# Kernel tuning notes

Measured on AMD Instinct MI355X. Metric: run time of the kernel, lower is better.

## Reference

```python
import jax, jax.numpy as jnp
import numpy as np

B, T, D, P = 32, 512, 256, 8
MEL_MAX = T * (P - 1)  # 3584, worst-case expanded length


def setup_inputs() -> dict:
    key = jax.random.key(0)
    k0, k1, k2 = jax.random.split(key, 3)
    x = jax.random.normal(k0, (B, T, D), dtype=jnp.float32)
    # Xavier-uniform-ish scaled weights
    W1 = jax.random.normal(k1, (D, D), dtype=jnp.float32) * (1.0 / np.sqrt(D))
    b1 = jnp.zeros((D,), dtype=jnp.float32)
    W2 = jax.random.normal(k2, (P, D), dtype=jnp.float32) * (1.0 / np.sqrt(D))
    b2 = jnp.zeros((P,), dtype=jnp.float32)
    return {"x": x, "W1": W1, "b1": b1, "W2": W2, "b2": b2,
            "mel_max_length": MEL_MAX}


def reference(x, W1, b1, W2, b2, mel_max_length):
    # DurationPredictor: Linear -> ReLU -> Linear -> softmax
    h = jax.nn.relu(jnp.einsum('btd,ed->bte', x, W1) + b1)
    P_probs = jax.nn.softmax(jnp.einsum('btd,pd->btp', h, W2) + b2, axis=-1)
    # transfer (eval): duration = argmax over class dim
    dur = jnp.argmax(P_probs, axis=-1)  # [B,T] ints in [0, P-1]; alpha=1.0
    # Vectorized LR/expand: frame t maps to the token whose cumulative
    # duration interval contains t.
    cs = jnp.cumsum(dur, axis=1)                 # [B,T] inclusive cumsum
    total = cs[:, -1]                            # [B] mel lengths
    t = jnp.arange(mel_max_length)               # [M]
    src = jax.vmap(lambda c: jnp.searchsorted(c, t, side='right'))(cs)  # [B,M]
    src = jnp.minimum(src, x.shape[1] - 1)
    out = jnp.take_along_axis(x, src[..., None], axis=1)  # [B,M,D]
    mask = (t[None, :] < total[:, None])[..., None]       # pad beyond length
    return jnp.where(mask, out, jnp.zeros((), dtype=x.dtype))
```

## Files before the change

### kernel.cpp

```cpp
#include <hip/hip_runtime.h>

#define B_ 32
#define T_ 512
#define D_ 256
#define P_ 8
#define BT (B_*T_)
#define ROWS 32
#define KT 32
#define NKT (D_/KT)

typedef float f4 __attribute__((ext_vector_type(4)));

__global__ void k_transpose(const float* __restrict__ W1, float* __restrict__ w1t) {
  int d = blockIdx.x;
  int e = threadIdx.x;
  w1t[d * D_ + e] = W1[e * D_ + d];
}

__global__ __launch_bounds__(256, 2) void k_dur(
    const float* __restrict__ x, const float* __restrict__ w1t,
    const float* __restrict__ b1, const float* __restrict__ W2,
    const float* __restrict__ b2, int* __restrict__ dur)
{
  __shared__ float xs[ROWS][D_];
  __shared__ float wst[KT][D_];

  const int tid  = threadIdx.x;
  const int lane = tid & 63;
  const int wave = tid >> 6;
  const int row0 = blockIdx.x * ROWS;

  for (int i = 0; i < 8; ++i) {
    int r = wave * 8 + i;
    const float* g = x + (size_t)(row0 + r) * D_ + lane * 4;
    __builtin_amdgcn_global_load_lds(
        (const __attribute__((address_space(1))) void*)g,
        (__attribute__((address_space(3))) void*)&xs[r][0], 16, 0, 0);
  }

  f4 b1v = *(const f4*)(b1 + lane * 4);
  f4 acc[8];
  #pragma unroll
  for (int i = 0; i < 8; ++i) acc[i] = b1v;

  for (int kt = 0; kt < NKT; ++kt) {
    for (int i = 0; i < 8; ++i) {
      int dd = wave * 8 + i;
      const float* g = w1t + (size_t)(kt * KT + dd) * D_ + lane * 4;
      __builtin_amdgcn_global_load_lds(
          (const __attribute__((address_space(1))) void*)g,
          (__attribute__((address_space(3))) void*)&wst[dd][0], 16, 0, 0);
    }
    __syncthreads();

    f4 loc[8];
    #pragma unroll
    for (int i = 0; i < 8; ++i) loc[i] = (f4){0.f, 0.f, 0.f, 0.f};

    #pragma unroll
    for (int dq = 0; dq < KT / 4; ++dq) {
      f4 wv[4];
      #pragma unroll
      for (int j = 0; j < 4; ++j) wv[j] = *(const f4*)&wst[dq * 4 + j][lane * 4];
      #pragma unroll
      for (int i = 0; i < 8; ++i) {
        f4 xv = *(const f4*)&xs[wave * 8 + i][kt * KT + dq * 4];
        loc[i] += xv.x * wv[0];
        loc[i] += xv.y * wv[1];
        loc[i] += xv.z * wv[2];
        loc[i] += xv.w * wv[3];
      }
    }
    #pragma unroll
    for (int i = 0; i < 8; ++i) acc[i] += loc[i];
    __syncthreads();
  }

  #pragma unroll
  for (int i = 0; i < 8; ++i)
    #pragma unroll
    for (int c = 0; c < 4; ++c) acc[i][c] = fmaxf(acc[i][c], 0.f);

  f4 w2r[P_];
  #pragma unroll
  for (int p = 0; p < P_; ++p) w2r[p] = *(const f4*)(W2 + p * D_ + lane * 4);
  float b2r[P_];
  #pragma unroll
  for (int p = 0; p < P_; ++p) b2r[p] = b2[p];

  float v[64];
  #pragma unroll
  for (int r = 0; r < 8; ++r)
    #pragma unroll
    for (int p = 0; p < P_; ++p) {
      f4 h = acc[r];
      v[r * 8 + p] = h[0]*w2r[p][0] + h[1]*w2r[p][1] + h[2]*w2r[p][2] + h[3]*w2r[p][3];
    }

  #pragma unroll
  for (int step = 0; step < 3; ++step) {
    const int s = 1 << step;
    const int half = 32 >> step;
    const bool upper = (lane & s) != 0;
    #pragma unroll
    for (int i = 0; i < half; ++i) {
      float a = v[i], b = v[i + half];
      float send = upper ? a : b;
      float recv = __shfl_xor(send, s, 64);
      v[i] = (upper ? b : a) + recv;
    }
  }
  #pragma unroll
  for (int s = 8; s < 64; s <<= 1)
    #pragma unroll
    for (int i = 0; i < 8; ++i) v[i] += __shfl_xor(v[i], s, 64);

  if (lane < 8) {
    float best = v[0] + b2r[0];
    int am = 0;
    #pragma unroll
    for (int p = 1; p < P_; ++p) {
      float L = v[p] + b2r[p];
      if (L > best) { best = L; am = p; }
    }
    int r = ((lane & 1) << 2) | (lane & 2) | ((lane & 4) >> 2);
    dur[row0 + wave * 8 + r] = am;
  }
}

__global__ void k_scan(const int* __restrict__ dur, int* __restrict__ src, int mel) {
  __shared__ int sh[T_];
  int t = threadIdx.x, b = blockIdx.x;
  int d = dur[b * T_ + t];
  sh[t] = d;
  __syncthreads();
  for (int s = 1; s < T_; s <<= 1) {
    int a = (t >= s) ? sh[t - s] : 0;
    __syncthreads();
    sh[t] += a;
    __syncthreads();
  }
  int cs = sh[t];
  int start = cs - d;
  int total = sh[T_ - 1];
  for (int m = start; m < cs; ++m) src[b * mel + m] = t;
  for (int m = total + t; m < mel; m += T_) src[b * mel + m] = -1;
}

__global__ __launch_bounds__(256) void k_gather(
    const float* __restrict__ x, const int* __restrict__ src,
    float* __restrict__ out, int mel)
{
  int lane = threadIdx.x & 63;
  int wave = threadIdx.x >> 6;
  int m = blockIdx.x * 4 + wave;
  int b = blockIdx.y;
  if (m >= mel) return;
  int s = src[b * mel + m];
  f4 val = {0.f, 0.f, 0.f, 0.f};
  if (s >= 0) val = *(const f4*)(x + ((size_t)b * T_ + s) * D_ + lane * 4);
  *(f4*)(out + ((size_t)b * mel + m) * D_ + lane * 4) = val;
}

extern "C" void kernel_launch(void* const* d_in, const int* in_sizes, int n_in,
                              void* d_out, int out_size, void* d_ws, size_t ws_size,
                              hipStream_t stream) {
  const float* x  = (const float*)d_in[0];
  const float* W1 = (const float*)d_in[1];
  const float* b1 = (const float*)d_in[2];
  const float* W2 = (const float*)d_in[3];
  const float* b2 = (const float*)d_in[4];
  float* out = (float*)d_out;

  int mel = out_size / (B_ * D_);

  float* w1t = (float*)d_ws;
  int*   dur = (int*)((char*)d_ws + D_ * D_ * sizeof(float));
  int*   src = dur + BT;

  k_transpose<<<D_, D_, 0, stream>>>(W1, w1t);
  k_dur<<<BT / ROWS, 256, 0, stream>>>(x, w1t, b1, W2, b2, dur);
  k_scan<<<B_, T_, 0, stream>>>(dur, src, mel);
  k_gather<<<dim3((mel + 3) / 4, B_), 256, 0, stream>>>(x, src, out, mel);
}
```

Baseline: 69.81 us.

## Double-buffer W1 tiles, double rows per block, and use wave-shuffle scan

The duration kernel now processes 64 rows per block (16 per wave) and double-buffers the W1 tile in LDS, prefetching tile kt+2 while computing tile kt with explicit vmcnt waits and raw barriers. This raises weight reuse per LDS load and overlaps global-to-LDS transfers with the FMA loop. Register and LDS use go up (occupancy hint drops to 1 block/CU) and the grid halves to 256 blocks. The scan kernel replaces the LDS Hillis-Steele loop with a wavefront shuffle scan plus a small per-wave sum fix-up, cutting barriers.

After: 203.3 us. 191% more time.

```diff
diff --git a/kernel.cpp b/kernel.cpp
--- a/kernel.cpp
+++ b/kernel.cpp
@@ -5,9 +5,10 @@
 #define D_ 256
 #define P_ 8
 #define BT (B_*T_)
-#define ROWS 32
 #define KT 32
 #define NKT (D_/KT)
+#define RPW 16
+#define RPB 64
 
 typedef float f4 __attribute__((ext_vector_type(4)));
 
@@ -17,54 +18,57 @@
   w1t[d * D_ + e] = W1[e * D_ + d];
 }
 
-__global__ __launch_bounds__(256, 2) void k_dur(
+__global__ __launch_bounds__(256, 1) void k_dur(
     const float* __restrict__ x, const float* __restrict__ w1t,
     const float* __restrict__ b1, const float* __restrict__ W2,
     const float* __restrict__ b2, int* __restrict__ dur)
 {
-  __shared__ float xs[ROWS][D_];
-  __shared__ float wst[KT][D_];
+  __shared__ float xs[RPB][D_];
+  __shared__ float wst[2][KT][D_];
 
   const int tid  = threadIdx.x;
   const int lane = tid & 63;
   const int wave = tid >> 6;
-  const int row0 = blockIdx.x * ROWS;
-
-  for (int i = 0; i < 8; ++i) {
-    int r = wave * 8 + i;
+  const int row0 = blockIdx.x * RPB;
+
+  for (int i = 0; i < RPW; ++i) {
+    int r = wave * RPW + i;
     const float* g = x + (size_t)(row0 + r) * D_ + lane * 4;
     __builtin_amdgcn_global_load_lds(
         (const __attribute__((address_space(1))) void*)g,
         (__attribute__((address_space(3))) void*)&xs[r][0], 16, 0, 0);
   }
-
-  f4 b1v = *(const f4*)(b1 + lane * 4);
-  f4 acc[8];
-  #pragma unroll
-  for (int i = 0; i < 8; ++i) acc[i] = b1v;
-
-  for (int kt = 0; kt < NKT; ++kt) {
+  for (int bu = 0; bu < 2; ++bu)
     for (int i = 0; i < 8; ++i) {
       int dd = wave * 8 + i;
-      const float* g = w1t + (size_t)(kt * KT + dd) * D_ + lane * 4;
+      const float* g = w1t + (size_t)(bu * KT + dd) * D_ + lane * 4;
       __builtin_amdgcn_global_load_lds(
           (const __attribute__((address_space(1))) void*)g,
-          (__attribute__((address_space(3))) void*)&wst[dd][0], 16, 0, 0);
-    }
-    __syncthreads();
-
-    f4 loc[8];
-    #pragma unroll
-    for (int i = 0; i < 8; ++i) loc[i] = (f4){0.f, 0.f, 0.f, 0.f};
+          (__attribute__((address_space(3))) void*)&wst[bu][dd][0], 16, 0, 0);
+    }
+  asm volatile("s_waitcnt vmcnt(8)" ::: "memory");
+  __builtin_amdgcn_s_barrier();
+  __builtin_amdgcn_sched_barrier(0);
+
+  f4 b1v = *(const f4*)(b1 + lane * 4);
+  f4 acc[RPW];
+  #pragma unroll
+  for (int i = 0; i < RPW; ++i) acc[i] = b1v;
+
+  for (int kt = 0; kt < NKT; ++kt) {
+    const int cur = kt & 1;
+    f4 loc[RPW];
+    #pragma unroll
+    for (int i = 0; i < RPW; ++i) loc[i] = (f4){0.f, 0.f, 0.f, 0.f};
 
     #pragma unroll
     for (int dq = 0; dq < KT / 4; ++dq) {
       f4 wv[4];
       #pragma unroll
-      for (int j = 0; j < 4; ++j) wv[j] = *(const f4*)&wst[dq * 4 + j][lane * 4];
-      #pragma unroll
-      for (int i = 0; i < 8; ++i) {
-        f4 xv = *(const f4*)&xs[wave * 8 + i][kt * KT + dq * 4];
+      for (int j = 0; j < 4; ++j) wv[j] = *(const f4*)&wst[cur][dq * 4 + j][lane * 4];
+      #pragma unroll
+      for (int i = 0; i < RPW; ++i) {
+        f4 xv = *(const f4*)&xs[wave * RPW + i][kt * KT + dq * 4];
         loc[i] += xv.x * wv[0];
         loc[i] += xv.y * wv[1];
         loc[i] += xv.z * wv[2];
@@ -72,12 +76,30 @@
       }
     }
     #pragma unroll
-    for (int i = 0; i < 8; ++i) acc[i] += loc[i];
-    __syncthreads();
-  }
-
-  #pragma unroll
-  for (int i = 0; i < 8; ++i)
+    for (int i = 0; i < RPW; ++i) acc[i] += loc[i];
+
+    if (kt < NKT - 1) {
+      __builtin_amdgcn_s_barrier();
+      __builtin_amdgcn_sched_barrier(0);
+      if (kt + 2 < NKT) {
+        for (int i = 0; i < 8; ++i) {
+          int dd = wave * 8 + i;
+          const float* g = w1t + (size_t)((kt + 2) * KT + dd) * D_ + lane * 4;
+          __builtin_amdgcn_global_load_lds(
+              (const __attribute__((address_space(1))) void*)g,
+              (__attribute__((address_space(3))) void*)&wst[cur][dd][0], 16, 0, 0);
+        }
+        asm volatile("s_waitcnt vmcnt(8)" ::: "memory");
+      } else {
+        asm volatile("s_waitcnt vmcnt(0)" ::: "memory");
+      }
+      __builtin_amdgcn_s_barrier();
+      __builtin_amdgcn_sched_barrier(0);
+    }
+  }
+
+  #pragma unroll
+  for (int i = 0; i < RPW; ++i)
     #pragma unroll
     for (int c = 0; c < 4; ++c) acc[i][c] = fmaxf(acc[i][c], 0.f);
 
@@ -88,61 +110,70 @@
   #pragma unroll
   for (int p = 0; p < P_; ++p) b2r[p] = b2[p];
 
-  float v[64];
-  #pragma unroll
-  for (int r = 0; r < 8; ++r)
-    #pragma unroll
-    for (int p = 0; p < P_; ++p) {
-      f4 h = acc[r];
-      v[r * 8 + p] = h[0]*w2r[p][0] + h[1]*w2r[p][1] + h[2]*w2r[p][2] + h[3]*w2r[p][3];
-    }
-
-  #pragma unroll
-  for (int step = 0; step < 3; ++step) {
-    const int s = 1 << step;
-    const int half = 32 >> step;
-    const bool upper = (lane & s) != 0;
-    #pragma unroll
-    for (int i = 0; i < half; ++i) {
-      float a = v[i], b = v[i + half];
-      float send = upper ? a : b;
-      float recv = __shfl_xor(send, s, 64);
-      v[i] = (upper ? b : a) + recv;
-    }
-  }
-  #pragma unroll
-  for (int s = 8; s < 64; s <<= 1)
-    #pragma unroll
-    for (int i = 0; i < 8; ++i) v[i] += __shfl_xor(v[i], s, 64);
-
-  if (lane < 8) {
-    float best = v[0] + b2r[0];
-    int am = 0;
-    #pragma unroll
-    for (int p = 1; p < P_; ++p) {
-      float L = v[p] + b2r[p];
-      if (L > best) { best = L; am = p; }
-    }
-    int r = ((lane & 1) << 2) | (lane & 2) | ((lane & 4) >> 2);
-    dur[row0 + wave * 8 + r] = am;
+  for (int half = 0; half < 2; ++half) {
+    float v[64];
+    #pragma unroll
+    for (int r = 0; r < 8; ++r)
+      #pragma unroll
+      for (int p = 0; p < P_; ++p) {
+        f4 h = acc[half * 8 + r];
+        v[r * 8 + p] = h[0]*w2r[p][0] + h[1]*w2r[p][1] + h[2]*w2r[p][2] + h[3]*w2r[p][3];
+      }
+
+    #pragma unroll
+    for (int step = 0; step < 3; ++step) {
+      const int s = 1 << step;
+      const int hl = 32 >> step;
+      const bool upper = (lane & s) != 0;
+      #pragma unroll
+      for (int i = 0; i < hl; ++i) {
+        float a = v[i], b = v[i + hl];
+        float send = upper ? a : b;
+        float recv = __shfl_xor(send, s, 64);
+        v[i] = (upper ? b : a) + recv;
+      }
+    }
+    #pragma unroll
+    for (int s = 8; s < 64; s <<= 1)
+      #pragma unroll
+      for (int i = 0; i < 8; ++i) v[i] += __shfl_xor(v[i], s, 64);
+
+    if (lane < 8) {
+      float best = v[0] + b2r[0];
+      int am = 0;
+      #pragma unroll
+      for (int p = 1; p < P_; ++p) {
+        float L = v[p] + b2r[p];
+        if (L > best) { best = L; am = p; }
+      }
+      int r = ((lane & 1) << 2) | (lane & 2) | ((lane & 4) >> 2);
+      dur[row0 + wave * RPW + half * 8 + r] = am;
+    }
   }
 }
 
 __global__ void k_scan(const int* __restrict__ dur, int* __restrict__ src, int mel) {
-  __shared__ int sh[T_];
+  __shared__ int wsum[8];
   int t = threadIdx.x, b = blockIdx.x;
+  int lane = t & 63, wave = t >> 6;
   int d = dur[b * T_ + t];
-  sh[t] = d;
+  int v = d;
+  #pragma unroll
+  for (int s = 1; s < 64; s <<= 1) {
+    int u = __shfl_up(v, s, 64);
+    if (lane >= s) v += u;
+  }
+  if (lane == 63) wsum[wave] = v;
   __syncthreads();
-  for (int s = 1; s < T_; s <<= 1) {
-    int a = (t >= s) ? sh[t - s] : 0;
-    __syncthreads();
-    sh[t] += a;
-    __syncthreads();
-  }
-  int cs = sh[t];
+  if (t == 0) {
+    int run = 0;
+    #pragma unroll
+    for (int i = 0; i < 8; ++i) { run += wsum[i]; wsum[i] = run; }
+  }
+  __syncthreads();
+  int cs = v + (wave ? wsum[wave - 1] : 0);
   int start = cs - d;
-  int total = sh[T_ - 1];
+  int total = wsum[7];
   for (int m = start; m < cs; ++m) src[b * mel + m] = t;
   for (int m = total + t; m < mel; m += T_) src[b * mel + m] = -1;
 }
@@ -179,7 +210,7 @@
   int*   src = dur + BT;
 
   k_transpose<<<D_, D_, 0, stream>>>(W1, w1t);
-  k_dur<<<BT / ROWS, 256, 0, stream>>>(x, w1t, b1, W2, b2, dur);
+  k_dur<<<BT / RPB, 256, 0, stream>>>(x, w1t, b1, W2, b2, dur);
   k_scan<<<B_, T_, 0, stream>>>(dur, src, mel);
   k_gather<<<dim3((mel + 3) / 4, B_), 256, 0, stream>>>(x, src, out, mel);
 }
```
